# Kernel optimization log

Measured on AMD Instinct MI355X. Metric: run time of the kernel, lower is better.

## Reference

```python
import jax, jax.numpy as jnp
import numpy as np

EPS = 1e-05

def _rms_norm(x, w, eps=EPS):
    xf = x.astype(jnp.float32)
    var = jnp.mean(xf * xf, axis=-1, keepdims=True)
    return (x * jax.lax.rsqrt(var + eps)) * w

def _apply_rotary_emb(x, freqs_cis):
    # x: [B,S,H,D], freqs_cis: [B,S,D] with cos in first half, sin in second
    half = freqs_cis.shape[-1] // 2
    cos = freqs_cis[..., :half][:, :, None, :]  # [B,S,1,D/2]
    sin = freqs_cis[..., half:][:, :, None, :]
    xf = x.astype(jnp.float32).reshape(*x.shape[:-1], -1, 2)
    xr, xi = xf[..., 0], xf[..., 1]
    out_r = xr * cos - xi * sin
    out_i = xr * sin + xi * cos
    out = jnp.stack([out_r, out_i], axis=-1).reshape(x.shape)
    return out.astype(x.dtype)

def setup_inputs() -> dict:
    key = jax.random.key(0)
    ks = jax.random.split(key, 8)
    B, S, D, H = 2, 4096, 2048, 16
    hd = D // H
    scale = 1.0 / np.sqrt(D)
    x = jax.random.normal(ks[0], (B, S, D), dtype=jnp.float32)
    freqs_cis = jax.random.normal(ks[1], (B, S, hd), dtype=jnp.float32)
    wq = jax.random.normal(ks[2], (D, D), dtype=jnp.float32) * scale
    wk = jax.random.normal(ks[3], (D, D), dtype=jnp.float32) * scale
    wv = jax.random.normal(ks[4], (D, D), dtype=jnp.float32) * scale
    wo = jax.random.normal(ks[5], (D, D), dtype=jnp.float32) * scale
    norm_q_w = jnp.ones((hd,), dtype=jnp.float32)
    norm_k_w = jnp.ones((hd,), dtype=jnp.float32)
    return {"x": x, "freqs_cis": freqs_cis, "wq": wq, "wk": wk, "wv": wv,
            "wo": wo, "norm_q_w": norm_q_w, "norm_k_w": norm_k_w}

def reference(x, freqs_cis, wq, wk, wv, wo, norm_q_w, norm_k_w):
    B, S, D = x.shape
    H = 16
    hd = D // H
    # Linear with torch convention: y = x @ W^T
    q = (x @ wq.T).reshape(B, S, H, hd)
    k = (x @ wk.T).reshape(B, S, H, hd)
    v = (x @ wv.T).reshape(B, S, H, hd)
    q = _rms_norm(q, norm_q_w)
    k = _rms_norm(k, norm_k_w)
    q = _apply_rotary_emb(q, freqs_cis)
    k = _apply_rotary_emb(k, freqs_cis)
    # SDPA: [B,H,S,hd]
    scale = 1.0 / jnp.sqrt(jnp.asarray(hd, dtype=jnp.float32))
    scores = jnp.einsum('bqhd,bkhd->bhqk', q, k) * scale
    attn = jax.nn.softmax(scores, axis=-1)
    out = jnp.einsum('bhqk,bkhd->bqhd', attn, v).reshape(B, S, D)
    return out @ wo.T
```

## Files before the change

### kernel.cpp

```cpp
#include <hip/hip_runtime.h>
#include <hip/hip_bf16.h>
#include <cstdint>
#include <cstdio>

typedef unsigned short ushort_t;
typedef __attribute__((ext_vector_type(8))) __bf16 bf16x8;
typedef __attribute__((ext_vector_type(2))) __bf16 bhalf2_t;
typedef __attribute__((ext_vector_type(8))) unsigned short us8;
typedef __attribute__((ext_vector_type(4))) unsigned short us4;
typedef __attribute__((ext_vector_type(4))) float f32x4;
typedef __attribute__((ext_vector_type(2))) float f32x2;

__device__ __forceinline__ ushort_t f2b(float f) {
  uint32_t u = __builtin_bit_cast(uint32_t, f);
  uint32_t r = (u + 0x7fffu + ((u >> 16) & 1u)) >> 16;
  return (ushort_t)r;
}
__device__ __forceinline__ float b2f(ushort_t s) {
  return __builtin_bit_cast(float, (uint32_t)s << 16);
}

__device__ __forceinline__ void gld_lds16(const void* g, void* l) {
  __builtin_amdgcn_global_load_lds(
      (__attribute__((address_space(1))) void*)(uintptr_t)g,
      (__attribute__((address_space(3))) void*)(uint32_t)(uintptr_t)l,
      16, 0, 0);
}

__global__ void cast_f2b(const float* __restrict__ src, ushort_t* __restrict__ dst, int n4) {
  int i = blockIdx.x * 256 + threadIdx.x;
  if (i < n4) {
    float4 f = ((const float4*)src)[i];
    us4 o = { f2b(f.x), f2b(f.y), f2b(f.z), f2b(f.w) };
    ((us4*)dst)[i] = o;
  }
}

__global__ void cast3_f2b(const float* __restrict__ a, const float* __restrict__ b,
                          const float* __restrict__ c, ushort_t* __restrict__ dst) {
  int i = blockIdx.x * 256 + threadIdx.x;
  int seg = i >> 20, local = i & 1048575;
  const float* src = (seg == 0) ? a : (seg == 1) ? b : c;
  float4 f = ((const float4*)src)[local];
  us4 o = { f2b(f.x), f2b(f.y), f2b(f.z), f2b(f.w) };
  ((us4*)dst)[i] = o;
}

#define LOAD_AH(AF, MH)                                                              \
  _Pragma("unroll")                                                                  \
  for (int kk = 0; kk < 2; ++kk) {                                                   \
    const int cx = ((kk * 4 + quad) ^ (m_l & 7)) * 8;                                \
    _Pragma("unroll")                                                                \
    for (int mt = 0; mt < 4; ++mt)                                                   \
      AF[kk][mt] = __builtin_bit_cast(bf16x8,                                        \
          *(const us8*)&Asc[(wr + ((MH) * 4 + mt) * 16 + m_l) * 64 + cx]);           \
  }
#define LOAD_BH(BF, NH)                                                              \
  _Pragma("unroll")                                                                  \
  for (int kk = 0; kk < 2; ++kk) {                                                   \
    const int cx = ((kk * 4 + quad) ^ (m_l & 7)) * 8;                                \
    _Pragma("unroll")                                                                \
    for (int nt = 0; nt < 2; ++nt)                                                   \
      BF[kk][nt] = __builtin_bit_cast(bf16x8,                                        \
          *(const us8*)&Bsc[(wc + ((NH) * 2 + nt) * 16 + m_l) * 64 + cx]);           \
  }
#define MFMA_QUAD(AF, BF, MH, NH)                                                    \
  _Pragma("unroll")                                                                  \
  for (int kk = 0; kk < 2; ++kk)                                                     \
    _Pragma("unroll")                                                                \
    for (int mt = 0; mt < 4; ++mt)                                                   \
      _Pragma("unroll")                                                              \
      for (int nt = 0; nt < 2; ++nt)                                                 \
        acc[(MH) * 4 + mt][(NH) * 2 + nt] = __builtin_amdgcn_mfma_f32_16x16x32_bf16( \
            AF[kk][mt], BF[kk][nt], acc[(MH) * 4 + mt][(NH) * 2 + nt], 0, 0, 0);

template <typename OutT>
__global__ __launch_bounds__(512, 2) void gemm_bt(const ushort_t* __restrict__ A,
                                                  const ushort_t* __restrict__ B,
                                                  OutT* __restrict__ C,
                                                  int M, int N, int K) {
  __shared__ ushort_t As0[256 * 64], As1[256 * 64];
  __shared__ ushort_t Bs0[256 * 64], Bs1[256 * 64];
  const int w    = threadIdx.x >> 6;
  const int lane = threadIdx.x & 63;
  const int m_l  = lane & 15;
  const int quad = lane >> 4;
  const int m0 = blockIdx.y * 256, n0 = blockIdx.x * 256;
  const int wr = (w >> 2) * 128, wc = (w & 3) * 64;

  f32x4 acc[8][4];
#pragma unroll
  for (int i = 0; i < 8; ++i)
#pragma unroll
    for (int j = 0; j < 4; ++j) acc[i][j] = (f32x4){0.f, 0.f, 0.f, 0.f};

  const int lr = lane >> 3;
  const int sc8 = ((lane & 7) ^ lr) * 8;
  const ushort_t* Abase = A + (size_t)(m0 + lr) * K + sc8;
  const ushort_t* Bbase = B + (size_t)(n0 + lr) * K + sc8;

  auto stageA = [&](ushort_t* dst, int kt, int h) {
#pragma unroll
    for (int t = 0; t < 2; ++t) {
      const int r0 = h * 128 + w * 16 + t * 8;
      gld_lds16(Abase + (size_t)r0 * K + (size_t)kt * 64, &dst[r0 * 64]);
    }
  };
  auto stageB = [&](ushort_t* dst, int kt, int h) {
#pragma unroll
    for (int t = 0; t < 2; ++t) {
      const int r0 = h * 128 + w * 16 + t * 8;
      gld_lds16(Bbase + (size_t)r0 * K + (size_t)kt * 64, &dst[r0 * 64]);
    }
  };

  const int ntile = K >> 6;

  stageA(As0, 0, 0); stageA(As0, 0, 1);
  stageB(Bs0, 0, 0); stageB(Bs0, 0, 1);
  if (ntile > 1) {
    stageA(As1, 1, 0); stageA(As1, 1, 1);
    asm volatile("s_waitcnt vmcnt(4)" ::: "memory");
  } else {
    asm volatile("s_waitcnt vmcnt(0)" ::: "memory");
  }
  __builtin_amdgcn_s_barrier();

  auto tileStep = [&](const ushort_t* Asc, const ushort_t* Bsc,
                      ushort_t* Asn, ushort_t* Bsn, int ti) {
    const bool pf = (ti + 1 < ntile);
    bf16x8 Af[2][4], Bf0[2][2], Bf1[2][2];
    LOAD_AH(Af, 0)
    LOAD_BH(Bf0, 0)
    if (pf) stageB(Bsn, ti + 1, 0);
    __builtin_amdgcn_s_barrier();
    __builtin_amdgcn_s_setprio(1);
    MFMA_QUAD(Af, Bf0, 0, 0)
    __builtin_amdgcn_s_setprio(0);
    __builtin_amdgcn_s_barrier();
    LOAD_BH(Bf1, 1)
    if (pf) stageB(Bsn, ti + 1, 1);
    __builtin_amdgcn_s_barrier();
    __builtin_amdgcn_s_setprio(1);
    MFMA_QUAD(Af, Bf1, 0, 1)
    __builtin_amdgcn_s_setprio(0);
    __builtin_amdgcn_s_barrier();
    LOAD_AH(Af, 1)
    __builtin_amdgcn_s_barrier();
    __builtin_amdgcn_s_setprio(1);
    MFMA_QUAD(Af, Bf1, 1, 1)
    MFMA_QUAD(Af, Bf0, 1, 0)
    __builtin_amdgcn_s_setprio(0);
    __builtin_amdgcn_s_barrier();
    if (ti + 2 < ntile) {
      stageA((ushort_t*)Asc, ti + 2, 0);
      stageA((ushort_t*)Asc, ti + 2, 1);
      asm volatile("s_waitcnt vmcnt(4)" ::: "memory");
      __builtin_amdgcn_s_barrier();
    } else if (ti + 1 < ntile) {
      asm volatile("s_waitcnt vmcnt(0)" ::: "memory");
      __builtin_amdgcn_s_barrier();
    }
  };

  for (int ti = 0; ti < ntile; ti += 2) {
    tileStep(As0, Bs0, As1, Bs1, ti);
    tileStep(As1, Bs1, As0, Bs0, ti + 1);
  }

#pragma unroll
  for (int mt = 0; mt < 8; ++mt)
#pragma unroll
    for (int nt = 0; nt < 4; ++nt)
#pragma unroll
      for (int r = 0; r < 4; ++r) {
        int row = m0 + wr + mt * 16 + quad * 4 + r;
        int col = n0 + wc + nt * 16 + m_l;
        float v = acc[mt][nt][r];
        if constexpr (__is_same(OutT, float)) C[(size_t)row * N + col] = v;
        else                                  C[(size_t)row * N + col] = f2b(v);
      }
}

__global__ void rmsrope(ushort_t* __restrict__ qkv, const float* __restrict__ freqs,
                        const float* __restrict__ wq, const float* __restrict__ wk) {
  int w = threadIdx.x >> 6, lane = threadIdx.x & 63;
  int rid = blockIdx.x * 4 + w;
  int h = rid & 15;
  int m = (rid >> 4) & 8191;
  int qk = rid >> 17;
  ushort_t* row = qkv + (size_t)m * 6144 + qk * 2048 + h * 128;
  uint32_t pr = *(const uint32_t*)(row + 2 * lane);
  float xr = b2f((ushort_t)(pr & 0xffff));
  float xi = b2f((ushort_t)(pr >> 16));
  float ss = xr * xr + xi * xi;
#pragma unroll
  for (int o = 1; o < 64; o <<= 1) ss += __shfl_xor(ss, o);
  float rinv = rsqrtf(ss * (1.f / 128.f) + 1e-5f);
  const float* wn = qk ? wk : wq;
  float nr = xr * rinv * wn[2 * lane];
  float ni = xi * rinv * wn[2 * lane + 1];
  float fc = freqs[(size_t)m * 128 + lane];
  float fs = freqs[(size_t)m * 128 + 64 + lane];
  float orr = nr * fc - ni * fs;
  float oii = nr * fs + ni * fc;
  const float k1 = 0.08838834764831845f * 1.4426950408889634f;
  float fscale = (qk == 0) ? k1 : 1.0f;
  orr *= fscale;
  oii *= fscale;
  *(uint32_t*)(row + 2 * lane) = (uint32_t)f2b(orr) | ((uint32_t)f2b(oii) << 16);
}

__global__ void transpose_v(const ushort_t* __restrict__ qkv, ushort_t* __restrict__ vt) {
  __shared__ ushort_t tile[64][136];
  int bh = blockIdx.y, s0 = blockIdx.x * 64;
  int b = bh >> 4, h = bh & 15;
  const ushort_t* src = qkv + (size_t)(b * 4096 + s0) * 6144 + 4096 + h * 128;
  int t = threadIdx.x;
  int r = t >> 2, c0 = (t & 3) * 32;
#pragma unroll
  for (int j = 0; j < 4; ++j)
    *(us8*)&tile[r][c0 + 8 * j] = *(const us8*)(src + (size_t)r * 6144 + c0 + 8 * j);
  __syncthreads();
  int d = t >> 1, sh = (t & 1) * 32;
  ushort_t* dst = vt + (size_t)bh * 524288 + (size_t)d * 4096 + s0 + sh;
#pragma unroll
  for (int i0 = 0; i0 < 32; i0 += 8) {
    us8 o;
#pragma unroll
    for (int j = 0; j < 8; ++j) o[j] = tile[sh + i0 + j][d];
    *(us8*)(dst + i0) = o;
  }
}

__global__ __launch_bounds__(256, 2) void flash_attn(const ushort_t* __restrict__ qkv,
                                                     const ushort_t* __restrict__ vt,
                                                     ushort_t* __restrict__ op0,
                                                     ushort_t* __restrict__ op1,
                                                     ushort_t* __restrict__ op2,
                                                     ushort_t* __restrict__ lbase) {
  __shared__ ushort_t Ks[2 * 64 * 128];
  __shared__ ushort_t VTs[2 * 128 * 64];

  const int w = threadIdx.x >> 6, lane = threadIdx.x & 63;
  const int m_l = lane & 15, quad = lane >> 4;

  const int id = blockIdx.x;
  const int xcd = id & 7, j = id >> 3;
  const int combo = xcd * 12 + (j >> 5);
  const int q0 = (j & 31) * 128;
  const int bh = combo & 31, split = combo >> 5;
  const int b = bh >> 4, h = bh & 15;
  const int kvbeg = split * 1344;
  const int kvend = (split == 2) ? 4096 : kvbeg + 1344;
  ushort_t* op = (split == 0) ? op0 : (split == 1) ? op1 : op2;

  const ushort_t* qb = qkv + (size_t)(b * 4096 + q0) * 6144 + h * 128;
  const ushort_t* kb = qkv + (size_t)(b * 4096) * 6144 + 2048 + h * 128;
  const ushort_t* vb = vt + (size_t)bh * 524288;

  const int lr = lane >> 4, p15 = lane & 15;

  bf16x8 qf[2][4];
  const int rowq = w * 16 + m_l;
  const int sqr = (m_l & 3) | ((m_l >> 3) << 2) | ((w & 1) << 3);
#pragma unroll
  for (int g = 0; g < 2; ++g) {
    __syncthreads();
#pragma unroll
    for (int t = 0; t < 4; ++t) {
      int rbase = w * 16 + t * 4;
      int sst = lr | ((t >> 1) << 2) | ((w & 1) << 3);
      gld_lds16(qb + (size_t)(g * 64 + rbase + lr) * 6144 + (p15 ^ sst) * 8, &Ks[rbase * 128]);
    }
    __syncthreads();
#pragma unroll
    for (int kk = 0; kk < 4; ++kk)
      qf[g][kk] = __builtin_bit_cast(bf16x8,
          *(const us8*)&Ks[rowq * 128 + ((kk * 4 + quad) ^ sqr) * 8]);
  }
  __syncthreads();

  int kbase[4];
#pragma unroll
  for (int mt = 0; mt < 4; ++mt)
    kbase[mt] = ((m_l >> 2) * 8 + (m_l & 3) + (mt & 1) * 4 + (mt >> 1) * 32) * 128;
  int cx[4];
#pragma unroll
  for (int kk = 0; kk < 4; ++kk) cx[kk] = ((kk * 4 + quad) ^ m_l) * 8;
  int vx[2];
#pragma unroll
  for (int kk = 0; kk < 2; ++kk) vx[kk] = ((kk * 4 + quad) ^ (m_l & 7)) * 8;

  auto issueKV = [&](int kv0, int bo) {
#pragma unroll
    for (int t = 0; t < 4; ++t) {
      int rbase = w * 16 + t * 4;
      int sst = lr | ((t >> 1) << 2) | ((w & 1) << 3);
      gld_lds16(kb + (size_t)(kv0 + rbase + lr) * 6144 + (p15 ^ sst) * 8, &Ks[bo + rbase * 128]);
    }
    int lr2 = lane >> 3, s2 = (lane & 7) ^ lr2;
#pragma unroll
    for (int t = 0; t < 4; ++t) {
      int r = w * 32 + t * 8;
      gld_lds16(vb + (size_t)(r + lr2) * 4096 + kv0 + s2 * 8, &VTs[bo + r * 64]);
    }
  };

  f32x4 lacc[2] = {(f32x4){0.f, 0.f, 0.f, 0.f}, (f32x4){0.f, 0.f, 0.f, 0.f}};
  f32x4 Oa[2][8];
#pragma unroll
  for (int g = 0; g < 2; ++g)
#pragma unroll
    for (int nt = 0; nt < 8; ++nt) Oa[g][nt] = (f32x4){0.f, 0.f, 0.f, 0.f};

  const int nit = (kvend - kvbeg) >> 6;
  issueKV(kvbeg, 0);

  for (int it = 0; it < nit; ++it) {
    const int kv0 = kvbeg + it * 64;
    const int bo = (it & 1) << 13;
    if (it + 1 < nit) {
      issueKV(kv0 + 64, bo ^ 8192);
      asm volatile("s_waitcnt vmcnt(8)" ::: "memory");
    } else {
      asm volatile("s_waitcnt vmcnt(0)" ::: "memory");
    }
    __builtin_amdgcn_s_barrier();

    f32x4 S[2][4];
#pragma unroll
    for (int g = 0; g < 2; ++g)
#pragma unroll
      for (int mt = 0; mt < 4; ++mt) S[g][mt] = (f32x4){0.f, 0.f, 0.f, 0.f};
    __builtin_amdgcn_s_setprio(1);
#pragma unroll
    for (int kk = 0; kk < 4; ++kk)
#pragma unroll
      for (int mt = 0; mt < 4; ++mt) {
        bf16x8 kf = __builtin_bit_cast(bf16x8, *(const us8*)&Ks[bo + kbase[mt] + cx[kk]]);
        S[0][mt] = __builtin_amdgcn_mfma_f32_16x16x32_bf16(kf, qf[0][kk], S[0][mt], 0, 0, 0);
        S[1][mt] = __builtin_amdgcn_mfma_f32_16x16x32_bf16(kf, qf[1][kk], S[1][mt], 0, 0, 0);
      }
    __builtin_amdgcn_s_setprio(0);

    union Upf { us8 u; bhalf2_t h[4]; } pf[2][2];
#pragma unroll
    for (int g = 0; g < 2; ++g) {
      f32x4 pe[4];
#pragma unroll
      for (int mt = 0; mt < 4; ++mt)
#pragma unroll
        for (int r = 0; r < 4; ++r)
          pe[mt][r] = __builtin_amdgcn_exp2f(S[g][mt][r]);
      lacc[g] += (pe[0] + pe[1]) + (pe[2] + pe[3]);
#pragma unroll
      for (int kk = 0; kk < 2; ++kk)
#pragma unroll
        for (int t = 0; t < 4; ++t) {
          int mt = kk * 2 + (t >> 1), r0 = (t & 1) * 2;
          f32x2 a = { pe[mt][r0], pe[mt][r0 + 1] };
          pf[g][kk].h[t] = __builtin_convertvector(a, bhalf2_t);
        }
    }

    __builtin_amdgcn_s_setprio(1);
#pragma unroll
    for (int kk = 0; kk < 2; ++kk) {
      bf16x8 p0 = __builtin_bit_cast(bf16x8, pf[0][kk].u);
      bf16x8 p1 = __builtin_bit_cast(bf16x8, pf[1][kk].u);
#pragma unroll
      for (int nt = 0; nt < 8; ++nt) {
        bf16x8 vf = __builtin_bit_cast(bf16x8,
            *(const us8*)&VTs[bo + (nt * 16 + m_l) * 64 + vx[kk]]);
        Oa[0][nt] = __builtin_amdgcn_mfma_f32_16x16x32_bf16(p0, vf, Oa[0][nt], 0, 0, 0);
        Oa[1][nt] = __builtin_amdgcn_mfma_f32_16x16x32_bf16(p1, vf, Oa[1][nt], 0, 0, 0);
      }
    }
    __builtin_amdgcn_s_setprio(0);
    __builtin_amdgcn_s_barrier();
  }

#pragma unroll
  for (int g = 0; g < 2; ++g) {
    float lsum = (lacc[g][0] + lacc[g][1]) + (lacc[g][2] + lacc[g][3]);
    lsum += __shfl_xor(lsum, 16);
    lsum += __shfl_xor(lsum, 32);
    if (quad == 0) {
      int s = q0 + g * 64 + w * 16 + m_l;
      *(float*)(lbase + (size_t)(b * 4096 + s) * 6144 + 4096 + h * 128 + split * 2) = lsum;
    }
#pragma unroll
    for (int r = 0; r < 4; ++r) {
      int s = q0 + g * 64 + w * 16 + quad * 4 + r;
      ushort_t* dst = op + (size_t)(b * 4096 + s) * 2048 + h * 128;
#pragma unroll
      for (int nt = 0; nt < 8; ++nt) dst[nt * 16 + m_l] = f2b(Oa[g][nt][r]);
    }
  }
}

__global__ void combine_splits(ushort_t* __restrict__ p0, const ushort_t* __restrict__ p1,
                               const ushort_t* __restrict__ p2, const ushort_t* __restrict__ lbase) {
  int tid = blockIdx.x * 256 + threadIdx.x;
  int row = tid >> 4;
  int brow = row >> 4, h = row & 15;
  const float* lp = (const float*)(lbase + (size_t)brow * 6144 + 4096 + h * 128);
  float inv = 1.f / (lp[0] + lp[1] + lp[2]);
  size_t off = (size_t)tid * 8;
  us8 a = *(const us8*)(p0 + off);
  us8 bb = *(const us8*)(p1 + off);
  us8 c = *(const us8*)(p2 + off);
  us8 o;
#pragma unroll
  for (int i = 0; i < 8; ++i)
    o[i] = f2b((b2f(a[i]) + b2f(bb[i]) + b2f(c[i])) * inv);
  *(us8*)(p0 + off) = o;
}

extern "C" void kernel_launch(void* const* d_in, const int* in_sizes, int n_in,
                              void* d_out, int out_size, void* d_ws, size_t ws_size,
                              hipStream_t stream) {
  const float* x     = (const float*)d_in[0];
  const float* freqs = (const float*)d_in[1];
  const float* wq    = (const float*)d_in[2];
  const float* wk    = (const float*)d_in[3];
  const float* wv    = (const float*)d_in[4];
  const float* wo    = (const float*)d_in[5];
  const float* nqw   = (const float*)d_in[6];
  const float* nkw   = (const float*)d_in[7];
  float* out = (float*)d_out;

  char* ws = (char*)d_ws;
  ushort_t* xb    = (ushort_t*)(ws);
  ushort_t* wqkvb = (ushort_t*)(ws + 33554432);
  ushort_t* qkvb  = (ushort_t*)(ws + 67108864);
  ushort_t* vtb   = (ushort_t*)(ws + 167772160);
  ushort_t* ctxb  = (ushort_t*)(ws + 201326592);
  ushort_t* part2 = wqkvb;
  ushort_t* wob2  = xb;
  if (ws_size < 234881024) { fprintf(stderr, "kernel_launch: ws too small (%zu < 234881024)\n", ws_size); return; }

  cast_f2b<<<16384, 256, 0, stream>>>(x, xb, 4194304);
  cast3_f2b<<<12288, 256, 0, stream>>>(wq, wk, wv, wqkvb);

  gemm_bt<ushort_t><<<dim3(24, 32), 512, 0, stream>>>(xb, wqkvb, qkvb, 8192, 6144, 2048);
  rmsrope<<<65536, 256, 0, stream>>>(qkvb, freqs, nqw, nkw);
  transpose_v<<<dim3(64, 32), 256, 0, stream>>>(qkvb, vtb);
  flash_attn<<<3072, 256, 0, stream>>>(qkvb, vtb, ctxb, xb, part2, qkvb);
  combine_splits<<<8192, 256, 0, stream>>>(ctxb, xb, part2, qkvb);
  cast_f2b<<<4096, 256, 0, stream>>>(wo, wob2, 1048576);
  gemm_bt<float><<<dim3(8, 32), 512, 0, stream>>>(ctxb, wob2, out, 8192, 2048, 2048);
}
```

Measured before the change: 751.2 us.

## Restructure GEMM main loop into 8-phase ping-pong with interleaved prefetch

```diff
diff --git a/kernel.cpp b/kernel.cpp
--- a/kernel.cpp
+++ b/kernel.cpp
@@ -46,23 +46,23 @@
   ((us4*)dst)[i] = o;
 }
 
-#define LOAD_AH(AF, MH)                                                              \
+#define LOAD_AH2(AF, AS, MH)                                                         \
   _Pragma("unroll")                                                                  \
   for (int kk = 0; kk < 2; ++kk) {                                                   \
     const int cx = ((kk * 4 + quad) ^ (m_l & 7)) * 8;                                \
     _Pragma("unroll")                                                                \
     for (int mt = 0; mt < 4; ++mt)                                                   \
       AF[kk][mt] = __builtin_bit_cast(bf16x8,                                        \
-          *(const us8*)&Asc[(wr + ((MH) * 4 + mt) * 16 + m_l) * 64 + cx]);           \
-  }
-#define LOAD_BH(BF, NH)                                                              \
+          *(const us8*)&AS[(wr + ((MH) * 4 + mt) * 16 + m_l) * 64 + cx]);            \
+  }
+#define LOAD_BH2(BF, BS, NH)                                                         \
   _Pragma("unroll")                                                                  \
   for (int kk = 0; kk < 2; ++kk) {                                                   \
     const int cx = ((kk * 4 + quad) ^ (m_l & 7)) * 8;                                \
     _Pragma("unroll")                                                                \
     for (int nt = 0; nt < 2; ++nt)                                                   \
       BF[kk][nt] = __builtin_bit_cast(bf16x8,                                        \
-          *(const us8*)&Bsc[(wc + ((NH) * 2 + nt) * 16 + m_l) * 64 + cx]);           \
+          *(const us8*)&BS[(wc + ((NH) * 2 + nt) * 16 + m_l) * 64 + cx]);            \
   }
 #define MFMA_QUAD(AF, BF, MH, NH)                                                    \
   _Pragma("unroll")                                                                  \
@@ -73,6 +73,13 @@
       for (int nt = 0; nt < 2; ++nt)                                                 \
         acc[(MH) * 4 + mt][(NH) * 2 + nt] = __builtin_amdgcn_mfma_f32_16x16x32_bf16( \
             AF[kk][mt], BF[kk][nt], acc[(MH) * 4 + mt][(NH) * 2 + nt], 0, 0, 0);
+#define PHASE(AF, BF, MH, NH, WAITCODE)                                              \
+  __builtin_amdgcn_s_barrier();                                                      \
+  __builtin_amdgcn_s_setprio(1);                                                     \
+  MFMA_QUAD(AF, BF, MH, NH)                                                          \
+  __builtin_amdgcn_s_setprio(0);                                                     \
+  WAITCODE                                                                           \
+  __builtin_amdgcn_s_barrier();
 
 template <typename OutT>
 __global__ __launch_bounds__(512, 2) void gemm_bt(const ushort_t* __restrict__ A,
@@ -118,54 +125,45 @@
 
   stageA(As0, 0, 0); stageA(As0, 0, 1);
   stageB(Bs0, 0, 0); stageB(Bs0, 0, 1);
-  if (ntile > 1) {
-    stageA(As1, 1, 0); stageA(As1, 1, 1);
-    asm volatile("s_waitcnt vmcnt(4)" ::: "memory");
-  } else {
-    asm volatile("s_waitcnt vmcnt(0)" ::: "memory");
-  }
+  stageB(Bs1, 1, 0); stageB(Bs1, 1, 1);
+  asm volatile("s_waitcnt vmcnt(4)" ::: "memory");
   __builtin_amdgcn_s_barrier();
 
-  auto tileStep = [&](const ushort_t* Asc, const ushort_t* Bsc,
-                      ushort_t* Asn, ushort_t* Bsn, int ti) {
-    const bool pf = (ti + 1 < ntile);
+  for (int ti = 0; ti < ntile; ti += 2) {
+    const bool s2 = (ti + 2 < ntile);
     bf16x8 Af[2][4], Bf0[2][2], Bf1[2][2];
-    LOAD_AH(Af, 0)
-    LOAD_BH(Bf0, 0)
-    if (pf) stageB(Bsn, ti + 1, 0);
-    __builtin_amdgcn_s_barrier();
-    __builtin_amdgcn_s_setprio(1);
-    MFMA_QUAD(Af, Bf0, 0, 0)
-    __builtin_amdgcn_s_setprio(0);
-    __builtin_amdgcn_s_barrier();
-    LOAD_BH(Bf1, 1)
-    if (pf) stageB(Bsn, ti + 1, 1);
-    __builtin_amdgcn_s_barrier();
-    __builtin_amdgcn_s_setprio(1);
-    MFMA_QUAD(Af, Bf1, 0, 1)
-    __builtin_amdgcn_s_setprio(0);
-    __builtin_amdgcn_s_barrier();
-    LOAD_AH(Af, 1)
-    __builtin_amdgcn_s_barrier();
-    __builtin_amdgcn_s_setprio(1);
-    MFMA_QUAD(Af, Bf1, 1, 1)
-    MFMA_QUAD(Af, Bf0, 1, 0)
-    __builtin_amdgcn_s_setprio(0);
-    __builtin_amdgcn_s_barrier();
-    if (ti + 2 < ntile) {
-      stageA((ushort_t*)Asc, ti + 2, 0);
-      stageA((ushort_t*)Asc, ti + 2, 1);
-      asm volatile("s_waitcnt vmcnt(4)" ::: "memory");
-      __builtin_amdgcn_s_barrier();
-    } else if (ti + 1 < ntile) {
-      asm volatile("s_waitcnt vmcnt(0)" ::: "memory");
-      __builtin_amdgcn_s_barrier();
-    }
-  };
-
-  for (int ti = 0; ti < ntile; ti += 2) {
-    tileStep(As0, Bs0, As1, Bs1, ti);
-    tileStep(As1, Bs1, As0, Bs0, ti + 1);
+    LOAD_AH2(Af, As0, 0)
+    LOAD_BH2(Bf0, Bs0, 0)
+    stageA(As1, ti + 1, 0);
+    PHASE(Af, Bf0, 0, 0, )
+    LOAD_BH2(Bf1, Bs0, 1)
+    stageA(As1, ti + 1, 1);
+    PHASE(Af, Bf1, 0, 1, )
+    LOAD_AH2(Af, As0, 1)
+    if (s2) stageB(Bs0, ti + 2, 0);
+    PHASE(Af, Bf1, 1, 1, )
+    if (s2) stageB(Bs0, ti + 2, 1);
+    if (s2) {
+      PHASE(Af, Bf0, 1, 0, asm volatile("s_waitcnt vmcnt(4)" ::: "memory");)
+    } else {
+      PHASE(Af, Bf0, 1, 0, asm volatile("s_waitcnt vmcnt(0)" ::: "memory");)
+    }
+    LOAD_AH2(Af, As1, 0)
+    LOAD_BH2(Bf0, Bs1, 0)
+    if (s2) stageA(As0, ti + 2, 0);
+    PHASE(Af, Bf0, 0, 0, )
+    LOAD_BH2(Bf1, Bs1, 1)
+    if (s2) stageA(As0, ti + 2, 1);
+    PHASE(Af, Bf1, 0, 1, )
+    LOAD_AH2(Af, As1, 1)
+    if (s2) stageB(Bs1, ti + 3, 0);
+    PHASE(Af, Bf1, 1, 1, )
+    if (s2) stageB(Bs1, ti + 3, 1);
+    if (s2) {
+      PHASE(Af, Bf0, 1, 0, asm volatile("s_waitcnt vmcnt(4)" ::: "memory");)
+    } else {
+      PHASE(Af, Bf0, 1, 0, )
+    }
   }
 
 #pragma unroll
```

Result: slower. 789.6 us (+5.1%).
